# Kernel tuning notes

Hardware: AMD Instinct MI355X
Metric: run time of the kernel (lower is better)

## Reference

```python
import jax, jax.numpy as jnp
import numpy as np

B, N, C, D = 1, 8192, 256, 128
MASK_VAL = jnp.float32(-1e16)


def setup_inputs() -> dict:
    key = jax.random.key(0)
    k_in, k_g, k_w, k_b = jax.random.split(key, 4)
    inputs = jax.random.normal(k_in, (B, N, C), dtype=jnp.float32)
    # row has at least one unmasked entry (standard GAT practice).
    graph = (jax.random.uniform(k_g, (N, N)) < 0.01).astype(jnp.float32)
    graph = jnp.maximum(graph, jnp.eye(N, dtype=jnp.float32))
    W = jax.random.normal(k_w, (D, C), dtype=jnp.float32)  # nn.Linear weight [out,in]
    b = jax.random.normal(k_b, (D,), dtype=jnp.float32)
    return {"inputs": inputs, "graph": graph, "W": W, "b": b}


def reference(inputs, graph, W, b):
    # h = W(inputs): [B,N,D]
    h = jnp.einsum('bnc,dc->bnd', inputs, W)
    # dense scores masked by adjacency: [B,N,N]
    scores = jnp.einsum('bnd,bmd->bnm', h, h) * graph[None, :, :]
    # torch: masked_fill_(scores == 0, -1e16)
    scores = jnp.where(scores == 0.0, MASK_VAL, scores)
    attention = jax.nn.softmax(scores, axis=2)
    return jnp.einsum('bnm,bmd->bnd', attention, h) + b
```

## Files before the change

kernel.cpp:

```cpp
#include <hip/hip_runtime.h>
#include <math.h>

#define Nn 8192
#define Cc 256
#define Dd 128
#define CAP 192

typedef float fx4 __attribute__((ext_vector_type(4)));

__global__ __launch_bounds__(256) void h_kernel(const float* __restrict__ x,
                                                const float* __restrict__ W,
                                                float* __restrict__ h) {
  __shared__ float xs[32 * Cc];
  const int tid = threadIdx.x;
  const int row0 = blockIdx.x * 32;
  const float4* xg4 = (const float4*)(x + (size_t)row0 * Cc);
  float4* xs4 = (float4*)xs;
#pragma unroll
  for (int k = 0; k < 8; ++k) xs4[tid + k * 256] = xg4[tid + k * 256];
  __syncthreads();

  const int d = tid & 127;
  const int g = tid >> 7;
  const float4* w4 = (const float4*)(W + (size_t)d * Cc);
  const float4* xt = (const float4*)(xs + g * 16 * Cc);

  float acc[16];
#pragma unroll
  for (int r = 0; r < 16; ++r) acc[r] = 0.f;

#pragma unroll 2
  for (int c4 = 0; c4 < Cc / 4; ++c4) {
    const float4 w = w4[c4];
#pragma unroll
    for (int r = 0; r < 16; ++r) {
      const float4 a = xt[r * (Cc / 4) + c4];
      acc[r] += a.x * w.x + a.y * w.y + a.z * w.z + a.w * w.w;
    }
  }
  const int rbase = row0 + g * 16;
#pragma unroll
  for (int r = 0; r < 16; ++r) {
    h[(size_t)(rbase + r) * Dd + d] = acc[r];
  }
}

__global__ __launch_bounds__(256) void scan_kernel(const float* __restrict__ graph,
                                                   int* __restrict__ counts,
                                                   int* __restrict__ edges) {
  __shared__ int idxs[4][CAP];
  const int wv   = threadIdx.x >> 6;
  const int lane = threadIdx.x & 63;
  const int i = blockIdx.x * 4 + wv;
  int* idx = idxs[wv];

  const fx4* row = (const fx4*)(graph + (size_t)i * Nn);
  const unsigned long long lmask = (1ull << lane) - 1ull;
  int cnt = 0;

#pragma unroll
  for (int c = 0; c < 4; ++c) {
    fx4 v[8];
#pragma unroll
    for (int t = 0; t < 8; ++t)
      v[t] = __builtin_nontemporal_load(&row[(c * 8 + t) * 64 + lane]);
#pragma unroll
    for (int t = 0; t < 8; ++t) {
      const int col = 4 * ((c * 8 + t) * 64 + lane);
      {
        const unsigned long long mk = __ballot(v[t].x != 0.f);
        const int p = cnt + __popcll(mk & lmask);
        if (v[t].x != 0.f && p < CAP) idx[p] = col + 0;
        cnt += __popcll(mk);
      }
      {
        const unsigned long long mk = __ballot(v[t].y != 0.f);
        const int p = cnt + __popcll(mk & lmask);
        if (v[t].y != 0.f && p < CAP) idx[p] = col + 1;
        cnt += __popcll(mk);
      }
      {
        const unsigned long long mk = __ballot(v[t].z != 0.f);
        const int p = cnt + __popcll(mk & lmask);
        if (v[t].z != 0.f && p < CAP) idx[p] = col + 2;
        cnt += __popcll(mk);
      }
      {
        const unsigned long long mk = __ballot(v[t].w != 0.f);
        const int p = cnt + __popcll(mk & lmask);
        if (v[t].w != 0.f && p < CAP) idx[p] = col + 3;
        cnt += __popcll(mk);
      }
    }
  }
  const int m = min(cnt, CAP);
  for (int e = lane; e < m; e += 64) edges[(size_t)i * CAP + e] = idx[e];
  if (lane == 0) counts[i] = m;
}

__global__ __launch_bounds__(256) void attn_kernel(const int* __restrict__ counts,
                                                   const int* __restrict__ edges,
                                                   const float* __restrict__ h,
                                                   const float* __restrict__ bias,
                                                   float* __restrict__ out) {
  __shared__ int   idxs[4][CAP];
  __shared__ float scs[4][CAP];
  __shared__ float his[4][Dd];
  const int wv   = threadIdx.x >> 6;
  const int lane = threadIdx.x & 63;
  const int i = blockIdx.x * 4 + wv;
  int*   idx = idxs[wv];
  float* sc  = scs[wv];
  float* hi  = his[wv];

  const int m = counts[i];
  *(float2*)(hi + lane * 2) = *(const float2*)(h + (size_t)i * Dd + lane * 2);

  const int* erow = edges + (size_t)i * CAP;
  for (int e = lane; e < m; e += 64) idx[e] = erow[e];

  const float4* h4 = (const float4*)hi;
  for (int e = lane; e < m; e += 64) {
    const int j = idx[e];
    const float4* hj = (const float4*)(h + (size_t)j * Dd);
    float s0 = 0.f, s1 = 0.f, s2 = 0.f, s3 = 0.f;
#pragma unroll
    for (int k = 0; k < Dd / 4; ++k) {
      const float4 a = h4[k];
      const float4 b = hj[k];
      s0 += a.x * b.x; s1 += a.y * b.y; s2 += a.z * b.z; s3 += a.w * b.w;
    }
    sc[e] = (s0 + s1) + (s2 + s3);
  }

  float lmax = -INFINITY;
  for (int e = lane; e < m; e += 64) {
    const float s = sc[e];
    if (s != 0.f) lmax = fmaxf(lmax, s);
  }
#pragma unroll
  for (int off = 32; off > 0; off >>= 1) lmax = fmaxf(lmax, __shfl_xor(lmax, off));

  float lsum = 0.f;
  for (int e = lane; e < m; e += 64) {
    const float s = sc[e];
    const float p = (s != 0.f) ? __expf(s - lmax) : 0.f;
    sc[e] = p;
    lsum += p;
  }
#pragma unroll
  for (int off = 32; off > 0; off >>= 1) lsum += __shfl_xor(lsum, off);
  const float inv = 1.f / lsum;

  float accx = 0.f, accy = 0.f;
#pragma unroll 8
  for (int e = 0; e < m; ++e) {
    const float p = sc[e];
    const int j = idx[e];
    const float2 hv = *(const float2*)(h + (size_t)j * Dd + lane * 2);
    accx += p * hv.x;
    accy += p * hv.y;
  }
  const float2 bv = *(const float2*)(bias + lane * 2);
  float2 o;
  o.x = accx * inv + bv.x;
  o.y = accy * inv + bv.y;
  *(float2*)(out + (size_t)i * Dd + lane * 2) = o;
}

extern "C" void kernel_launch(void* const* d_in, const int* in_sizes, int n_in,
                              void* d_out, int out_size, void* d_ws, size_t ws_size,
                              hipStream_t stream) {
  const float* x     = (const float*)d_in[0];
  const float* graph = (const float*)d_in[1];
  const float* W     = (const float*)d_in[2];
  const float* bias  = (const float*)d_in[3];
  float* out = (float*)d_out;

  float* h      = (float*)d_ws;
  int*   counts = (int*)((char*)d_ws + (size_t)Nn * Dd * 4);
  int*   edges  = counts + Nn;

  h_kernel<<<Nn / 32, 256, 0, stream>>>(x, W, h);
  scan_kernel<<<Nn / 4, 256, 0, stream>>>(graph, counts, edges);
  attn_kernel<<<Nn / 4, 256, 0, stream>>>(counts, edges, h, bias, out);
}
```

Before: 485.4 us.

## Fuse attention into single-pass online softmax and simplify projection kernel

```diff
diff --git a/kernel.cpp b/kernel.cpp
--- a/kernel.cpp
+++ b/kernel.cpp
@@ -11,38 +11,34 @@
 __global__ __launch_bounds__(256) void h_kernel(const float* __restrict__ x,
                                                 const float* __restrict__ W,
                                                 float* __restrict__ h) {
-  __shared__ float xs[32 * Cc];
   const int tid = threadIdx.x;
-  const int row0 = blockIdx.x * 32;
-  const float4* xg4 = (const float4*)(x + (size_t)row0 * Cc);
-  float4* xs4 = (float4*)xs;
-#pragma unroll
-  for (int k = 0; k < 8; ++k) xs4[tid + k * 256] = xg4[tid + k * 256];
-  __syncthreads();
+  const int d = tid & 127;
+  const int rhalf = tid >> 7;
+  const int row0 = blockIdx.x * 8 + rhalf * 4;
 
-  const int d = tid & 127;
-  const int g = tid >> 7;
   const float4* w4 = (const float4*)(W + (size_t)d * Cc);
-  const float4* xt = (const float4*)(xs + g * 16 * Cc);
+  const float4* x0 = (const float4*)(x + (size_t)(row0 + 0) * Cc);
+  const float4* x1 = (const float4*)(x + (size_t)(row0 + 1) * Cc);
+  const float4* x2 = (const float4*)(x + (size_t)(row0 + 2) * Cc);
+  const float4* x3 = (const float4*)(x + (size_t)(row0 + 3) * Cc);
 
-  float acc[16];
-#pragma unroll
-  for (int r = 0; r < 16; ++r) acc[r] = 0.f;
-
-#pragma unroll 2
+  float a0 = 0.f, a1 = 0.f, a2 = 0.f, a3 = 0.f;
+#pragma unroll 8
   for (int c4 = 0; c4 < Cc / 4; ++c4) {
     const float4 w = w4[c4];
-#pragma unroll
-    for (int r = 0; r < 16; ++r) {
-      const float4 a = xt[r * (Cc / 4) + c4];
-      acc[r] += a.x * w.x + a.y * w.y + a.z * w.z + a.w * w.w;
-    }
+    const float4 u0 = x0[c4];
+    const float4 u1 = x1[c4];
+    const float4 u2 = x2[c4];
+    const float4 u3 = x3[c4];
+    a0 += u0.x * w.x + u0.y * w.y + u0.z * w.z + u0.w * w.w;
+    a1 += u1.x * w.x + u1.y * w.y + u1.z * w.z + u1.w * w.w;
+    a2 += u2.x * w.x + u2.y * w.y + u2.z * w.z + u2.w * w.w;
+    a3 += u3.x * w.x + u3.y * w.y + u3.z * w.z + u3.w * w.w;
   }
-  const int rbase = row0 + g * 16;
-#pragma unroll
-  for (int r = 0; r < 16; ++r) {
-    h[(size_t)(rbase + r) * Dd + d] = acc[r];
-  }
+  h[(size_t)(row0 + 0) * Dd + d] = a0;
+  h[(size_t)(row0 + 1) * Dd + d] = a1;
+  h[(size_t)(row0 + 2) * Dd + d] = a2;
+  h[(size_t)(row0 + 3) * Dd + d] = a3;
 }
 
 __global__ __launch_bounds__(256) void scan_kernel(const float* __restrict__ graph,
@@ -103,64 +99,53 @@
                                                    const float* __restrict__ h,
                                                    const float* __restrict__ bias,
                                                    float* __restrict__ out) {
-  __shared__ int   idxs[4][CAP];
-  __shared__ float scs[4][CAP];
-  __shared__ float his[4][Dd];
   const int wv   = threadIdx.x >> 6;
   const int lane = threadIdx.x & 63;
   const int i = blockIdx.x * 4 + wv;
-  int*   idx = idxs[wv];
-  float* sc  = scs[wv];
-  float* hi  = his[wv];
 
   const int m = counts[i];
-  *(float2*)(hi + lane * 2) = *(const float2*)(h + (size_t)i * Dd + lane * 2);
+  const float2 hi2 = *(const float2*)(h + (size_t)i * Dd + lane * 2);
+  const int* erow = edges + (size_t)i * CAP;
 
-  const int* erow = edges + (size_t)i * CAP;
-  for (int e = lane; e < m; e += 64) idx[e] = erow[e];
+  float M = -INFINITY, L = 0.f;
+  float accx = 0.f, accy = 0.f;
 
-  const float4* h4 = (const float4*)hi;
-  for (int e = lane; e < m; e += 64) {
-    const int j = idx[e];
-    const float4* hj = (const float4*)(h + (size_t)j * Dd);
-    float s0 = 0.f, s1 = 0.f, s2 = 0.f, s3 = 0.f;
+  for (int base = 0; base < m; base += 64) {
+    const int nb = min(64, m - base);
+    const int jv = (lane < nb) ? erow[base + lane] : i;
+
+    for (int e0 = 0; e0 < nb; e0 += 8) {
+      const int ne = min(8, nb - e0);
+      float2 hv[8];
 #pragma unroll
-    for (int k = 0; k < Dd / 4; ++k) {
-      const float4 a = h4[k];
-      const float4 b = hj[k];
-      s0 += a.x * b.x; s1 += a.y * b.y; s2 += a.z * b.z; s3 += a.w * b.w;
+      for (int t = 0; t < 8; ++t) {
+        if (t < ne) {
+          const int j = __shfl(jv, e0 + t);
+          hv[t] = *(const float2*)(h + (size_t)j * Dd + lane * 2);
+        }
+      }
+#pragma unroll
+      for (int t = 0; t < 8; ++t) {
+        if (t < ne) {
+          float pd = hi2.x * hv[t].x + hi2.y * hv[t].y;
+#pragma unroll
+          for (int off = 32; off > 0; off >>= 1) pd += __shfl_xor(pd, off);
+          const float s = pd;
+          if (s != 0.f) {
+            const float newM = fmaxf(M, s);
+            const float scale = __expf(M - newM);
+            const float p = __expf(s - newM);
+            L = L * scale + p;
+            accx = accx * scale + p * hv[t].x;
+            accy = accy * scale + p * hv[t].y;
+            M = newM;
+          }
+        }
+      }
     }
-    sc[e] = (s0 + s1) + (s2 + s3);
   }
 
-  float lmax = -INFINITY;
-  for (int e = lane; e < m; e += 64) {
-    const float s = sc[e];
-    if (s != 0.f) lmax = fmaxf(lmax, s);
-  }
-#pragma unroll
-  for (int off = 32; off > 0; off >>= 1) lmax = fmaxf(lmax, __shfl_xor(lmax, off));
-
-  float lsum = 0.f;
-  for (int e = lane; e < m; e += 64) {
-    const float s = sc[e];
-    const float p = (s != 0.f) ? __expf(s - lmax) : 0.f;
-    sc[e] = p;
-    lsum += p;
-  }
-#pragma unroll
-  for (int off = 32; off > 0; off >>= 1) lsum += __shfl_xor(lsum, off);
-  const float inv = 1.f / lsum;
-
-  float accx = 0.f, accy = 0.f;
-#pragma unroll 8
-  for (int e = 0; e < m; ++e) {
-    const float p = sc[e];
-    const int j = idx[e];
-    const float2 hv = *(const float2*)(h + (size_t)j * Dd + lane * 2);
-    accx += p * hv.x;
-    accy += p * hv.y;
-  }
+  const float inv = 1.f / L;
   const float2 bv = *(const float2*)(bias + lane * 2);
   float2 o;
   o.x = accx * inv + bv.x;
@@ -181,7 +166,7 @@
   int*   counts = (int*)((char*)d_ws + (size_t)Nn * Dd * 4);
   int*   edges  = counts + Nn;
 
-  h_kernel<<<Nn / 32, 256, 0, stream>>>(x, W, h);
+  h_kernel<<<Nn / 8, 256, 0, stream>>>(x, W, h);
   scan_kernel<<<Nn / 4, 256, 0, stream>>>(graph, counts, edges);
   attn_kernel<<<Nn / 4, 256, 0, stream>>>(counts, edges, h, bias, out);
 }
```

Measured after the change: 491.5 us. About the same (+1.3%).
